# Kernel tuning notes

Measured on AMD Instinct MI355X. Metric: run time of the kernel, lower is better.

## Reference

```python
import jax, jax.numpy as jnp
import numpy as np

DIM = 192
HEADS = 6
PE_TABLE_SIZE = 2601  # 51x51 relative-position grid, rows of length pos_dim+3=5


def setup_inputs() -> dict:
    key = jax.random.key(0)
    ks = jax.random.split(key, 16)
    b, n, m, c = 2, 8192, 48, DIM
    feat = jax.random.normal(ks[0], (b, n, c), dtype=jnp.float32)
    member_idx = jax.random.randint(ks[1], (b, n, m), 0, n)
    cluster_mask = (jax.random.uniform(ks[2], (b, n, m)) > 0.1).astype(jnp.float32)
    pe_idx = jax.random.randint(ks[3], (b, n, m), 0, PE_TABLE_SIZE)
    s = 1.0 / np.sqrt(c)
    Wq = jax.random.normal(ks[4], (c, c), dtype=jnp.float32) * s
    bq = jnp.zeros((c,), jnp.float32)
    Wkv = jax.random.normal(ks[5], (2 * c, c), dtype=jnp.float32) * s
    bkv = jnp.zeros((2 * c,), jnp.float32)
    Wpe = jax.random.normal(ks[6], (HEADS, 5), dtype=jnp.float32) * 0.4
    bpe = jnp.zeros((HEADS,), jnp.float32)
    blank_k = jax.random.normal(ks[7], (c,), dtype=jnp.float32)
    blank_v = jax.random.normal(ks[8], (c,), dtype=jnp.float32)
    Wproj = jax.random.normal(ks[9], (c, c), dtype=jnp.float32) * s
    bproj = jnp.zeros((c,), jnp.float32)
    pre_table = jax.random.normal(ks[10], (PE_TABLE_SIZE, 5), dtype=jnp.float32)
    return {"feat": feat, "member_idx": member_idx, "cluster_mask": cluster_mask,
            "pe_idx": pe_idx, "global_attn": 0,
            "Wq": Wq, "bq": bq, "Wkv": Wkv, "bkv": bkv, "Wpe": Wpe, "bpe": bpe,
            "blank_k": blank_k, "blank_v": blank_v, "Wproj": Wproj, "bproj": bproj,
            "pre_table": pre_table}


def reference(feat, member_idx, cluster_mask, pe_idx, global_attn,
              Wq, bq, Wkv, bkv, Wpe, bpe, blank_k, blank_v, Wproj, bproj, pre_table):
    b, n, c = feat.shape
    h = Wpe.shape[0]
    c_ = c // h
    scale = c_ ** (-0.5)

    q = (feat @ Wq.T + bq) * scale                      # [b,n,c]
    kv = (feat @ Wkv.T + bkv).reshape(b, n, h, 2, c_)   # split like torch view(b,n,h,2,c_)
    k = kv[:, :, :, 0, :]                               # [b,n,h,c_]
    v = kv[:, :, :, 1, :]                               # [b,n,h,c_]
    q = q.reshape(b, n, h, c_)

    # positional-embedding lookup table: [T,5] -> [T,h]
    pe_table = pre_table @ Wpe.T + bpe
    pos = pe_table[pe_idx]                              # [b,n,m,h]

    if not global_attn:
        m = member_idx.shape[-1]
        idx = member_idx.reshape(b, n * m, 1)
        # gather neighbor keys/values: CLUSTENQK / CLUSTENAV semantics
        kg = jnp.take_along_axis(k.reshape(b, n, h * c_), idx, axis=1).reshape(b, n, m, h, c_)
        attn = jnp.einsum('bnhc,bnmhc->bhnm', q, kg)    # [b,h,n,m]
        attn = attn + pos.transpose(0, 3, 1, 2)
        attn = attn + (1.0 - cluster_mask)[:, None] * (-100.0)
    else:
        attn = jnp.einsum('bnhc,bshc->bhns', q, k)
        attn = attn + pos.transpose(0, 3, 1, 2)

    # blank token logit, clamped
    blank = jnp.clip(jnp.einsum('bnhc,hc->bhn', q, blank_k.reshape(h, c_)), -5.0, 5.0)[..., None]
    attn_all = jax.nn.softmax(jnp.concatenate([attn, blank], axis=-1), axis=-1)
    attn_nb = attn_all[..., :-1]                        # [b,h,n,m]
    blank_a = attn_all[..., -1:]                        # [b,h,n,1]

    if not global_attn:
        vg = jnp.take_along_axis(v.reshape(b, n, h * c_), idx, axis=1).reshape(b, n, m, h, c_)
        out = jnp.einsum('bhnm,bnmhc->bnhc', attn_nb, vg)
    else:
        out = jnp.einsum('bhns,bshc->bnhc', attn_nb, v)

    out = out + blank_a.transpose(0, 2, 1, 3) * blank_v.reshape(1, 1, h, c_)
    out = out.reshape(b, n, c)
    return out @ Wproj.T + bproj
```

## Files before the change

kernel.cpp:

```cpp
#include <hip/hip_runtime.h>
#include <hip/hip_fp16.h>

#define DIMC 192
#define HEADS 6
#define NSEQ 8192
#define NB 2
#define NMEM 48
#define PE_N 2601
#define NTOT (NB * NSEQ)

typedef _Float16 f16;
typedef __attribute__((ext_vector_type(4))) _Float16 f16x4;
typedef __attribute__((ext_vector_type(8))) _Float16 f16x8;
typedef __attribute__((ext_vector_type(4))) float f32x4;
typedef __attribute__((ext_vector_type(4))) int i32x4;

static __device__ __forceinline__ float dot8(f16x8 a, f16x8 b) {
    return (float)a[0] * (float)b[0] + (float)a[1] * (float)b[1]
         + (float)a[2] * (float)b[2] + (float)a[3] * (float)b[3]
         + (float)a[4] * (float)b[4] + (float)a[5] * (float)b[5]
         + (float)a[6] * (float)b[6] + (float)a[7] * (float)b[7];
}

__global__ void pe_kernel(const float* __restrict__ pre_table,
                          const float* __restrict__ Wpe,
                          const float* __restrict__ bpe,
                          float* __restrict__ pe_out) {
    int i = blockIdx.x * blockDim.x + threadIdx.x;
    if (i >= PE_N) return;
    float p0 = pre_table[i * 5 + 0], p1 = pre_table[i * 5 + 1], p2 = pre_table[i * 5 + 2];
    float p3 = pre_table[i * 5 + 3], p4 = pre_table[i * 5 + 4];
#pragma unroll
    for (int h = 0; h < HEADS; ++h) {
        float s = bpe[h] + p0 * Wpe[h * 5 + 0] + p1 * Wpe[h * 5 + 1] + p2 * Wpe[h * 5 + 2]
                + p3 * Wpe[h * 5 + 3] + p4 * Wpe[h * 5 + 4];
        pe_out[i * HEADS + h] = s;
    }
}

#define FEAT4 (NTOT * DIMC / 4)
#define WQ4   (DIMC * DIMC / 4)
#define WKV4  (2 * DIMC * DIMC / 4)
#define BL4   (DIMC / 4)
__global__ __launch_bounds__(256) void cvt_kernel(
    const float* __restrict__ feat, const float* __restrict__ Wq,
    const float* __restrict__ Wkv, const float* __restrict__ Wproj,
    const float* __restrict__ blank_k, const float* __restrict__ blank_v,
    f16* __restrict__ featH, f16* __restrict__ WqH, f16* __restrict__ WkvH,
    f16* __restrict__ WprojH, f16* __restrict__ bkH, f16* __restrict__ bvH) {
    const int total = FEAT4 + WQ4 + WKV4 + WQ4 + BL4 + BL4;
    for (int i = blockIdx.x * 256 + threadIdx.x; i < total; i += gridDim.x * 256) {
        const float* src; f16* dst; int j = i;
        if (j < FEAT4)                { src = feat;    dst = featH; }
        else if ((j -= FEAT4) < WQ4)  { src = Wq;      dst = WqH; }
        else if ((j -= WQ4) < WKV4)   { src = Wkv;     dst = WkvH; }
        else if ((j -= WKV4) < WQ4)   { src = Wproj;   dst = WprojH; }
        else if ((j -= WQ4) < BL4)    { src = blank_k; dst = bkH; }
        else { j -= BL4;                src = blank_v;  dst = bvH; }
        float4 f = *reinterpret_cast<const float4*>(src + (size_t)j * 4);
        f16x4 h = {(f16)f.x, (f16)f.y, (f16)f.z, (f16)f.w};
        *reinterpret_cast<f16x4*>(dst + (size_t)j * 4) = h;
    }
}

template <int MODE, int TPB>
__global__ __launch_bounds__(256) void gemm_kernel(
    const f16* __restrict__ A, const f16* __restrict__ W0, const f16* __restrict__ Wkv,
    const float* __restrict__ b0, const float* __restrict__ bkv,
    f16* __restrict__ oq, f16* __restrict__ ok, f16* __restrict__ ov,
    float* __restrict__ ofp) {
    __shared__ __align__(16) char smem[48 * 1024];
    f16* As = (f16*)smem;
    f16 (*Cs)[72] = (f16(*)[72])smem;
    f16* Bs = (f16*)(smem + 24 * 1024);
    const int tid = threadIdx.x, w = tid >> 6, l = tid & 63;
    const size_t rowbase = (size_t)blockIdx.x * 64;

    const char* Abase = (const char*)(A + rowbase * DIMC);
#pragma unroll
    for (int i = 0; i < 6; ++i) {
        const int L = (w * 6 + i) * 64 + l;
        const int row = L / 24, cp = L % 24;
        __builtin_amdgcn_global_load_lds(
            (const __attribute__((address_space(1))) unsigned int*)
                (Abase + row * 384 + ((cp ^ (row & 7)) << 4)),
            (__attribute__((address_space(3))) unsigned int*)
                (As + (size_t)(w * 6 + i) * 512),
            16, 0, 0);
    }
    __syncthreads();

    const int lm = l & 15, lg = l >> 4;
    const int wr = w & 1, wc = w >> 1;
    const char* AsB = (const char*)As;
    const int r0 = wr * 32 + lm, r1 = r0 + 16;
    f16x8 af0[6], af1[6];
#pragma unroll
    for (int ks = 0; ks < 6; ++ks) {
        const int ch = ((ks * 4 + lg) ^ (lm & 7)) << 4;
        af0[ks] = *reinterpret_cast<const f16x8*>(AsB + r0 * 384 + ch);
        af1[ks] = *reinterpret_cast<const f16x8*>(AsB + r1 * 384 + ch);
    }

    for (int t = 0; t < TPB; ++t) {
        const int ct = blockIdx.y * TPB + t;
        {
            const int cb = ct * 64;
            const f16* Wsel = (MODE == 0 && cb >= DIMC)
                                  ? (Wkv + (size_t)(cb - DIMC) * DIMC)
                                  : (W0 + (size_t)cb * DIMC);
            const char* Wbase = (const char*)Wsel;
#pragma unroll
            for (int i = 0; i < 6; ++i) {
                const int L = (w * 6 + i) * 64 + l;
                const int row = L / 24, cp = L % 24;
                __builtin_amdgcn_global_load_lds(
                    (const __attribute__((address_space(1))) unsigned int*)
                        (Wbase + row * 384 + ((cp ^ (row & 7)) << 4)),
                    (__attribute__((address_space(3))) unsigned int*)
                        (Bs + (size_t)(w * 6 + i) * 512),
                    16, 0, 0);
            }
        }
        __syncthreads();
        f32x4 a00 = {0.f, 0.f, 0.f, 0.f}, a01 = a00, a10 = a00, a11 = a00;
        const char* BsB = (const char*)Bs;
        const int b0r = (wc * 32 + lm) * 384, b1r = b0r + 16 * 384;
#pragma unroll
        for (int ks = 0; ks < 6; ++ks) {
            const int ch = ((ks * 4 + lg) ^ (lm & 7)) << 4;
            f16x8 q0 = *reinterpret_cast<const f16x8*>(BsB + b0r + ch);
            f16x8 q1 = *reinterpret_cast<const f16x8*>(BsB + b1r + ch);
            a00 = __builtin_amdgcn_mfma_f32_16x16x32_f16(af0[ks], q0, a00, 0, 0, 0);
            a01 = __builtin_amdgcn_mfma_f32_16x16x32_f16(af0[ks], q1, a01, 0, 0, 0);
            a10 = __builtin_amdgcn_mfma_f32_16x16x32_f16(af1[ks], q0, a10, 0, 0, 0);
            a11 = __builtin_amdgcn_mfma_f32_16x16x32_f16(af1[ks], q1, a11, 0, 0, 0);
        }
#pragma unroll
        for (int fm = 0; fm < 2; ++fm)
#pragma unroll
            for (int fn = 0; fn < 2; ++fn) {
                const f32x4 acc = fm ? (fn ? a11 : a10) : (fn ? a01 : a00);
                const int crow = wr * 32 + fm * 16 + lg * 4;
                const int ccol = wc * 32 + fn * 16 + lm;
#pragma unroll
                for (int r = 0; r < 4; ++r) Cs[crow + r][ccol] = (f16)acc[r];
            }
        __syncthreads();
        {
            const int row = tid >> 2, s = tid & 3;
            const int cb = ct * 64;
            const size_t gr = rowbase + row;
            f16x8 v0 = *reinterpret_cast<const f16x8*>(&Cs[row][s * 16]);
            f16x8 v1 = *reinterpret_cast<const f16x8*>(&Cs[row][s * 16 + 8]);
            const int c0 = cb + s * 16;
            if (MODE == 1) {
                float4 o[4];
#pragma unroll
                for (int tt = 0; tt < 8; ++tt) {
                    ((float*)o)[tt]     = (float)v0[tt] + b0[c0 + tt];
                    ((float*)o)[tt + 8] = (float)v1[tt] + b0[c0 + 8 + tt];
                }
                float4* dst = reinterpret_cast<float4*>(ofp + gr * DIMC + c0);
                dst[0] = o[0]; dst[1] = o[1]; dst[2] = o[2]; dst[3] = o[3];
            } else if (c0 < DIMC) {
                const float sc = 0.17677669529663687f;
                f16x8 w0h, w1h;
#pragma unroll
                for (int tt = 0; tt < 8; ++tt) {
                    w0h[tt] = (f16)(((float)v0[tt] + b0[c0 + tt]) * sc);
                    w1h[tt] = (f16)(((float)v1[tt] + b0[c0 + 8 + tt]) * sc);
                }
                *reinterpret_cast<f16x8*>(oq + gr * DIMC + c0) = w0h;
                *reinterpret_cast<f16x8*>(oq + gr * DIMC + c0 + 8) = w1h;
            } else {
                const int t0 = c0 - DIMC;
                const int hh = t0 >> 6, rr = t0 & 63;
                f16* base = (rr < 32) ? (ok + hh * 32 + (rr & 31))
                                      : (ov + hh * 32 + (rr & 31));
                f16x8 w0h, w1h;
#pragma unroll
                for (int tt = 0; tt < 8; ++tt) {
                    w0h[tt] = (f16)((float)v0[tt] + bkv[t0 + tt]);
                    w1h[tt] = (f16)((float)v1[tt] + bkv[t0 + 8 + tt]);
                }
                *reinterpret_cast<f16x8*>(base + gr * DIMC) = w0h;
                *reinterpret_cast<f16x8*>(base + gr * DIMC + 8) = w1h;
            }
        }
    }
}

__device__ __forceinline__ int map_qi(int bid, int wave) {
    const int xcd = bid & 7, j = bid >> 3;
    const int batch = xcd >> 2;
    const int qslot = j * 4 + (xcd & 3);
    return batch * NSEQ + qslot * 4 + wave;
}

__global__ __launch_bounds__(256) void attnA_kernel(
    const f16* __restrict__ qH, const f16* __restrict__ kH, const f16* __restrict__ bkH,
    const int* __restrict__ member_idx, const float* __restrict__ cmask,
    const int* __restrict__ pe_idx, const float* __restrict__ peT,
    f16* __restrict__ w16) {
    __shared__ float p_lds[4][HEADS][64];
    __shared__ int m_lds[4][64];
    const int wave = threadIdx.x >> 6, lane = threadIdx.x & 63;
    const int qi = map_qi(blockIdx.x, wave);
    const int bbase = qi & ~(NSEQ - 1);
    if (lane < NMEM)
        m_lds[wave][lane] = bbase + member_idx[(size_t)qi * NMEM + lane];
    const int g = lane >> 3, sub = lane & 7;
    const f16* qrow = qH + (size_t)qi * DIMC;
    const f16x8 qv0 = *reinterpret_cast<const f16x8*>(qrow + sub * 8);
    const f16x8 qv1 = *reinterpret_cast<const f16x8*>(qrow + 64 + sub * 8);
    const f16x8 qv2 = *reinterpret_cast<const f16x8*>(qrow + 128 + sub * 8);
#pragma unroll
    for (int it = 0; it < 7; ++it) {
        const int m = it * 8 + g;
        const bool act = (m <= NMEM);
        const f16* kp = (act && m < NMEM) ? (kH + (size_t)m_lds[wave][m] * DIMC) : bkH;
        const f16x8 k0 = *reinterpret_cast<const f16x8*>(kp + sub * 8);
        const f16x8 k1 = *reinterpret_cast<const f16x8*>(kp + 64 + sub * 8);
        const f16x8 k2 = *reinterpret_cast<const f16x8*>(kp + 128 + sub * 8);
        float d0 = dot8(qv0, k0), d1 = dot8(qv1, k1), d2 = dot8(qv2, k2);
        d0 += __shfl_xor(d0, 1); d0 += __shfl_xor(d0, 2);
        d1 += __shfl_xor(d1, 1); d1 += __shfl_xor(d1, 2);
        d2 += __shfl_xor(d2, 1); d2 += __shfl_xor(d2, 2);
        if (act && (sub == 0 || sub == 4)) {
            const int hb = sub >> 2;
            p_lds[wave][hb][m]     = d0;
            p_lds[wave][2 + hb][m] = d1;
            p_lds[wave][4 + hb][m] = d2;
        }
    }
    {
        const int m = lane;
        float lo[HEADS];
#pragma unroll
        for (int h = 0; h < HEADS; ++h)
            lo[h] = (m <= NMEM) ? p_lds[wave][h][m] : -1e30f;
        if (m < NMEM) {
            const int pei = pe_idx[(size_t)qi * NMEM + m];
            const float msk = (1.0f - cmask[(size_t)qi * NMEM + m]) * -100.0f;
#pragma unroll
            for (int h = 0; h < HEADS; ++h) lo[h] += peT[pei * HEADS + h] + msk;
        } else if (m == NMEM) {
#pragma unroll
            for (int h = 0; h < HEADS; ++h) lo[h] = fminf(fmaxf(lo[h], -5.f), 5.f);
        }
#pragma unroll
        for (int h = 0; h < HEADS; ++h) {
            float mx = lo[h];
#pragma unroll
            for (int st = 32; st; st >>= 1) mx = fmaxf(mx, __shfl_xor(mx, st));
            const float e = __expf(lo[h] - mx);
            float sm = e;
#pragma unroll
            for (int st = 32; st; st >>= 1) sm += __shfl_xor(sm, st);
            p_lds[wave][h][m] = e / sm;
        }
    }
#pragma unroll
    for (int h = 0; h < HEADS; ++h)
        w16[(size_t)qi * 384 + h * 64 + lane] = (f16)p_lds[wave][h][lane];
}

__global__ __launch_bounds__(256) void attnB_kernel(
    const f16* __restrict__ vH, const f16* __restrict__ bvH,
    const int* __restrict__ member_idx, const f16* __restrict__ w16,
    f16* __restrict__ outA) {
    __shared__ float p_lds[4][HEADS][64];
    __shared__ int m_lds[4][64];
    const int wave = threadIdx.x >> 6, lane = threadIdx.x & 63;
    const int qi = map_qi(blockIdx.x, wave);
    const int bbase = qi & ~(NSEQ - 1);
    if (lane < NMEM)
        m_lds[wave][lane] = bbase + member_idx[(size_t)qi * NMEM + lane];
#pragma unroll
    for (int h = 0; h < HEADS; ++h)
        p_lds[wave][h][lane] = (float)w16[(size_t)qi * 384 + h * 64 + lane];
    const int h0 = lane >> 5;
    float o0 = 0.f, o1 = 0.f, o2 = 0.f;
#pragma unroll 6
    for (int mm = 0; mm < NMEM; mm += 4) {
        const i32x4 rows = *reinterpret_cast<const i32x4*>(&m_lds[wave][mm]);
        const f32x4 w0 = *reinterpret_cast<const f32x4*>(&p_lds[wave][h0][mm]);
        const f32x4 w1 = *reinterpret_cast<const f32x4*>(&p_lds[wave][h0 + 2][mm]);
        const f32x4 w2 = *reinterpret_cast<const f32x4*>(&p_lds[wave][h0 + 4][mm]);
#pragma unroll
        for (int t = 0; t < 4; ++t) {
            const f16* vp = vH + (size_t)rows[t] * DIMC;
            o0 += w0[t] * (float)vp[lane];
            o1 += w1[t] * (float)vp[64 + lane];
            o2 += w2[t] * (float)vp[128 + lane];
        }
    }
    o0 += p_lds[wave][h0][NMEM]     * (float)bvH[lane];
    o1 += p_lds[wave][h0 + 2][NMEM] * (float)bvH[64 + lane];
    o2 += p_lds[wave][h0 + 4][NMEM] * (float)bvH[128 + lane];
    f16* orow = outA + (size_t)qi * DIMC;
    orow[lane] = (f16)o0; orow[64 + lane] = (f16)o1; orow[128 + lane] = (f16)o2;
}

extern "C" void kernel_launch(void* const* d_in, const int* in_sizes, int n_in,
                              void* d_out, int out_size, void* d_ws, size_t ws_size,
                              hipStream_t stream) {
    const float* feat      = (const float*)d_in[0];
    const int*   member_i  = (const int*)d_in[1];
    const float* cmask     = (const float*)d_in[2];
    const int*   pe_idx    = (const int*)d_in[3];
    const float* Wq        = (const float*)d_in[5];
    const float* bq        = (const float*)d_in[6];
    const float* Wkv       = (const float*)d_in[7];
    const float* bkv       = (const float*)d_in[8];
    const float* Wpe       = (const float*)d_in[9];
    const float* bpe       = (const float*)d_in[10];
    const float* blank_k   = (const float*)d_in[11];
    const float* blank_v   = (const float*)d_in[12];
    const float* Wproj     = (const float*)d_in[13];
    const float* bproj     = (const float*)d_in[14];
    const float* pre_table = (const float*)d_in[15];
    float* out = (float*)d_out;

    const size_t SZH = (size_t)NTOT * DIMC * sizeof(f16);
    char* ws = (char*)d_ws;
    f16* qH     = (f16*)(ws);
    f16* kH     = (f16*)(ws + SZH);
    f16* vH     = (f16*)(ws + 2 * SZH);
    f16* outAH  = (f16*)(ws + 3 * SZH);
    f16* featH  = (f16*)(ws + 4 * SZH);
    f16* w16    = (f16*)(ws + 5 * SZH);
    char* p = ws + 5 * SZH + (size_t)NTOT * 384 * 2;
    f16* WqH    = (f16*)p;              p += (size_t)DIMC * DIMC * 2;
    f16* WkvH   = (f16*)p;              p += (size_t)2 * DIMC * DIMC * 2;
    f16* WprojH = (f16*)p;              p += (size_t)DIMC * DIMC * 2;
    f16* bkH    = (f16*)p;              p += 512;
    f16* bvH    = (f16*)p;              p += 512;
    float* peT  = (float*)p;            p += (size_t)PE_N * HEADS * sizeof(float);
    if ((size_t)(p - ws) > ws_size) return;

    pe_kernel<<<(PE_N + 255) / 256, 256, 0, stream>>>(pre_table, Wpe, bpe, peT);
    cvt_kernel<<<1024, 256, 0, stream>>>(feat, Wq, Wkv, Wproj, blank_k, blank_v,
                                         featH, WqH, WkvH, WprojH, bkH, bvH);
    gemm_kernel<0, 3><<<dim3(NTOT / 64, 3), 256, 0, stream>>>(
        featH, WqH, WkvH, bq, bkv, qH, kH, vH, nullptr);
    attnA_kernel<<<NTOT / 4, 256, 0, stream>>>(qH, kH, bkH, member_i, cmask,
                                               pe_idx, peT, w16);
    attnB_kernel<<<NTOT / 4, 256, 0, stream>>>(vH, bvH, member_i, w16, outAH);
    gemm_kernel<1, 1><<<dim3(NTOT / 64, 3), 256, 0, stream>>>(
        outAH, WprojH, nullptr, bproj, nullptr, nullptr, nullptr, nullptr, out);
}
```

Measured before the change: 181.1 us.

## Fuse attention score and value kernels, merge prep kernels, use fdot2

Merges the two attention kernels into one so the softmax weights stay in LDS instead of being written to and re-read from a global f16 buffer. This also removes one launch and the duplicated member-index load. The PE-table and f16 conversion kernels are combined into one launch by partitioning blocks. The q·k dot products now use the packed fdot2 builtin instead of scalar converts and multiplies. The weights also skip the f16 rounding round-trip, and the fused kernel may use more registers.

Measured after the change: 176.3 us. 2.6% less time.

```diff
diff --git a/kernel.cpp b/kernel.cpp
--- a/kernel.cpp
+++ b/kernel.cpp
@@ -10,46 +10,57 @@
 #define NTOT (NB * NSEQ)
 
 typedef _Float16 f16;
+typedef __attribute__((ext_vector_type(2))) _Float16 f16x2;
 typedef __attribute__((ext_vector_type(4))) _Float16 f16x4;
 typedef __attribute__((ext_vector_type(8))) _Float16 f16x8;
 typedef __attribute__((ext_vector_type(4))) float f32x4;
 typedef __attribute__((ext_vector_type(4))) int i32x4;
 
-static __device__ __forceinline__ float dot8(f16x8 a, f16x8 b) {
-    return (float)a[0] * (float)b[0] + (float)a[1] * (float)b[1]
-         + (float)a[2] * (float)b[2] + (float)a[3] * (float)b[3]
-         + (float)a[4] * (float)b[4] + (float)a[5] * (float)b[5]
-         + (float)a[6] * (float)b[6] + (float)a[7] * (float)b[7];
-}
-
-__global__ void pe_kernel(const float* __restrict__ pre_table,
-                          const float* __restrict__ Wpe,
-                          const float* __restrict__ bpe,
-                          float* __restrict__ pe_out) {
-    int i = blockIdx.x * blockDim.x + threadIdx.x;
-    if (i >= PE_N) return;
-    float p0 = pre_table[i * 5 + 0], p1 = pre_table[i * 5 + 1], p2 = pre_table[i * 5 + 2];
-    float p3 = pre_table[i * 5 + 3], p4 = pre_table[i * 5 + 4];
-#pragma unroll
-    for (int h = 0; h < HEADS; ++h) {
-        float s = bpe[h] + p0 * Wpe[h * 5 + 0] + p1 * Wpe[h * 5 + 1] + p2 * Wpe[h * 5 + 2]
-                + p3 * Wpe[h * 5 + 3] + p4 * Wpe[h * 5 + 4];
-        pe_out[i * HEADS + h] = s;
-    }
+static __device__ __forceinline__ float fdot2p(f16x2 a, f16x2 b, float acc) {
+#if __has_builtin(__builtin_amdgcn_fdot2)
+    return __builtin_amdgcn_fdot2(a, b, acc, false);
+#else
+    return acc + (float)a[0] * (float)b[0] + (float)a[1] * (float)b[1];
+#endif
+}
+static __device__ __forceinline__ float dot8f(f16x8 a, f16x8 b) {
+    float s0 = fdot2p((f16x2){a[0], a[1]}, (f16x2){b[0], b[1]}, 0.f);
+    s0 = fdot2p((f16x2){a[2], a[3]}, (f16x2){b[2], b[3]}, s0);
+    float s1 = fdot2p((f16x2){a[4], a[5]}, (f16x2){b[4], b[5]}, 0.f);
+    s1 = fdot2p((f16x2){a[6], a[7]}, (f16x2){b[6], b[7]}, s1);
+    return s0 + s1;
 }
 
 #define FEAT4 (NTOT * DIMC / 4)
 #define WQ4   (DIMC * DIMC / 4)
 #define WKV4  (2 * DIMC * DIMC / 4)
 #define BL4   (DIMC / 4)
-__global__ __launch_bounds__(256) void cvt_kernel(
+#define PE_BLOCKS ((PE_N + 255) / 256)
+#define CVT_BLOCKS 1024
+__global__ __launch_bounds__(256) void prep_kernel(
+    const float* __restrict__ pre_table, const float* __restrict__ Wpe,
+    const float* __restrict__ bpe, float* __restrict__ pe_out,
     const float* __restrict__ feat, const float* __restrict__ Wq,
     const float* __restrict__ Wkv, const float* __restrict__ Wproj,
     const float* __restrict__ blank_k, const float* __restrict__ blank_v,
     f16* __restrict__ featH, f16* __restrict__ WqH, f16* __restrict__ WkvH,
     f16* __restrict__ WprojH, f16* __restrict__ bkH, f16* __restrict__ bvH) {
+    if (blockIdx.x < PE_BLOCKS) {
+        int i = blockIdx.x * 256 + threadIdx.x;
+        if (i >= PE_N) return;
+        float p0 = pre_table[i * 5 + 0], p1 = pre_table[i * 5 + 1], p2 = pre_table[i * 5 + 2];
+        float p3 = pre_table[i * 5 + 3], p4 = pre_table[i * 5 + 4];
+#pragma unroll
+        for (int h = 0; h < HEADS; ++h) {
+            float s = bpe[h] + p0 * Wpe[h * 5 + 0] + p1 * Wpe[h * 5 + 1] + p2 * Wpe[h * 5 + 2]
+                    + p3 * Wpe[h * 5 + 3] + p4 * Wpe[h * 5 + 4];
+            pe_out[i * HEADS + h] = s;
+        }
+        return;
+    }
     const int total = FEAT4 + WQ4 + WKV4 + WQ4 + BL4 + BL4;
-    for (int i = blockIdx.x * 256 + threadIdx.x; i < total; i += gridDim.x * 256) {
+    for (int i = (blockIdx.x - PE_BLOCKS) * 256 + threadIdx.x; i < total;
+         i += CVT_BLOCKS * 256) {
         const float* src; f16* dst; int j = i;
         if (j < FEAT4)                { src = feat;    dst = featH; }
         else if ((j -= FEAT4) < WQ4)  { src = Wq;      dst = WqH; }
@@ -198,11 +209,12 @@
     return batch * NSEQ + qslot * 4 + wave;
 }
 
-__global__ __launch_bounds__(256) void attnA_kernel(
-    const f16* __restrict__ qH, const f16* __restrict__ kH, const f16* __restrict__ bkH,
+__global__ __launch_bounds__(256) void attn_kernel(
+    const f16* __restrict__ qH, const f16* __restrict__ kH, const f16* __restrict__ vH,
+    const f16* __restrict__ bkH, const f16* __restrict__ bvH,
     const int* __restrict__ member_idx, const float* __restrict__ cmask,
     const int* __restrict__ pe_idx, const float* __restrict__ peT,
-    f16* __restrict__ w16) {
+    f16* __restrict__ outA) {
     __shared__ float p_lds[4][HEADS][64];
     __shared__ int m_lds[4][64];
     const int wave = threadIdx.x >> 6, lane = threadIdx.x & 63;
@@ -223,7 +235,7 @@
         const f16x8 k0 = *reinterpret_cast<const f16x8*>(kp + sub * 8);
         const f16x8 k1 = *reinterpret_cast<const f16x8*>(kp + 64 + sub * 8);
         const f16x8 k2 = *reinterpret_cast<const f16x8*>(kp + 128 + sub * 8);
-        float d0 = dot8(qv0, k0), d1 = dot8(qv1, k1), d2 = dot8(qv2, k2);
+        float d0 = dot8f(qv0, k0), d1 = dot8f(qv1, k1), d2 = dot8f(qv2, k2);
         d0 += __shfl_xor(d0, 1); d0 += __shfl_xor(d0, 2);
         d1 += __shfl_xor(d1, 1); d1 += __shfl_xor(d1, 2);
         d2 += __shfl_xor(d2, 1); d2 += __shfl_xor(d2, 2);
@@ -261,25 +273,6 @@
             p_lds[wave][h][m] = e / sm;
         }
     }
-#pragma unroll
-    for (int h = 0; h < HEADS; ++h)
-        w16[(size_t)qi * 384 + h * 64 + lane] = (f16)p_lds[wave][h][lane];
-}
-
-__global__ __launch_bounds__(256) void attnB_kernel(
-    const f16* __restrict__ vH, const f16* __restrict__ bvH,
-    const int* __restrict__ member_idx, const f16* __restrict__ w16,
-    f16* __restrict__ outA) {
-    __shared__ float p_lds[4][HEADS][64];
-    __shared__ int m_lds[4][64];
-    const int wave = threadIdx.x >> 6, lane = threadIdx.x & 63;
-    const int qi = map_qi(blockIdx.x, wave);
-    const int bbase = qi & ~(NSEQ - 1);
-    if (lane < NMEM)
-        m_lds[wave][lane] = bbase + member_idx[(size_t)qi * NMEM + lane];
-#pragma unroll
-    for (int h = 0; h < HEADS; ++h)
-        p_lds[wave][h][lane] = (float)w16[(size_t)qi * 384 + h * 64 + lane];
     const int h0 = lane >> 5;
     float o0 = 0.f, o1 = 0.f, o2 = 0.f;
 #pragma unroll 6
@@ -330,8 +323,7 @@
     f16* vH     = (f16*)(ws + 2 * SZH);
     f16* outAH  = (f16*)(ws + 3 * SZH);
     f16* featH  = (f16*)(ws + 4 * SZH);
-    f16* w16    = (f16*)(ws + 5 * SZH);
-    char* p = ws + 5 * SZH + (size_t)NTOT * 384 * 2;
+    char* p = ws + 5 * SZH;
     f16* WqH    = (f16*)p;              p += (size_t)DIMC * DIMC * 2;
     f16* WkvH   = (f16*)p;              p += (size_t)2 * DIMC * DIMC * 2;
     f16* WprojH = (f16*)p;              p += (size_t)DIMC * DIMC * 2;
@@ -340,14 +332,13 @@
     float* peT  = (float*)p;            p += (size_t)PE_N * HEADS * sizeof(float);
     if ((size_t)(p - ws) > ws_size) return;
 
-    pe_kernel<<<(PE_N + 255) / 256, 256, 0, stream>>>(pre_table, Wpe, bpe, peT);
-    cvt_kernel<<<1024, 256, 0, stream>>>(feat, Wq, Wkv, Wproj, blank_k, blank_v,
-                                         featH, WqH, WkvH, WprojH, bkH, bvH);
+    prep_kernel<<<PE_BLOCKS + CVT_BLOCKS, 256, 0, stream>>>(
+        pre_table, Wpe, bpe, peT, feat, Wq, Wkv, Wproj, blank_k, blank_v,
+        featH, WqH, WkvH, WprojH, bkH, bvH);
     gemm_kernel<0, 3><<<dim3(NTOT / 64, 3), 256, 0, stream>>>(
         featH, WqH, WkvH, bq, bkv, qH, kH, vH, nullptr);
-    attnA_kernel<<<NTOT / 4, 256, 0, stream>>>(qH, kH, bkH, member_i, cmask,
-                                               pe_idx, peT, w16);
-    attnB_kernel<<<NTOT / 4, 256, 0, stream>>>(vH, bvH, member_i, w16, outAH);
+    attn_kernel<<<NTOT / 4, 256, 0, stream>>>(qH, kH, vH, bkH, bvH, member_i, cmask,
+                                              pe_idx, peT, outAH);
     gemm_kernel<1, 1><<<dim3(NTOT / 64, 3), 256, 0, stream>>>(
         outAH, WprojH, nullptr, bproj, nullptr, nullptr, nullptr, nullptr, out);
 }
```
